# Kernel tuning notes

Measured on AMD Instinct MI355X. Metric: run time of the kernel, lower is better.

Reference implementation:

```python
import jax, jax.numpy as jnp
import numpy as np

PAD, CLS, SEP, UNK = 0, 1, 2, 3
VOCAB, DIM, LATENT = 30000, 768, 5000
B, L, C = 16, 1024, 8


def setup_inputs() -> dict:
    key = jax.random.key(0)
    k1, k2, k3 = jax.random.split(key, 3)
    x = jax.random.randint(k1, (B, L, C), 0, VOCAB, dtype=jnp.int64)
    char_emb = jax.random.normal(k2, (VOCAB, DIM), dtype=jnp.float32)
    latent_mat = jax.random.normal(k3, (LATENT, DIM), dtype=jnp.float32) * (LATENT ** -0.5)
    return {"x": x, "char_emb": char_emb, "latent_mat": latent_mat}


def reference(x, char_emb, latent_mat):
    b, l, c = x.shape
    chars = x.reshape(-1, c)                       # (N, C)
    embs = char_emb[chars]                         # (N, C, D) gather
    pad_mask = chars == PAD                        # (N, C)
    embs = jnp.where(pad_mask[..., None], 0.0, embs)
    summed = embs.sum(axis=1)                      # (N, D)
    counts = jnp.clip((~pad_mask).sum(axis=-1), 1, None)  # (N,)
    lang_emb = jnp.tanh(summed / counts[:, None].astype(summed.dtype))  # (N, D)

    # soft codebook attention: matmul -> softmax -> matmul
    scores = jnp.einsum('nd,kd->nk', lang_emb, latent_mat)   # (N, LATENT)
    dist = jax.nn.softmax(scores, axis=-1)
    latent_emb = jnp.einsum('nk,kd->nd', dist, latent_mat)    # (N, D)
    sde = lang_emb + latent_emb

    # special-token overwrite based on first char id
    first = chars[:, 0]
    for tid in (PAD, UNK, SEP, CLS):
        sde = jnp.where((first == tid)[:, None], char_emb[tid], sde)
    return sde.reshape(b, l, -1)
```

## Files before the change

kernel.cpp:

```cpp
#include <hip/hip_runtime.h>

#define PAD_ID 0
#define NTOK   16384
#define DIM    768
#define KLAT   5000
#define KPAD   5024
#define NSTEP  157
#define TILE_SH 24576
#define TOKB   32

typedef float f32x4 __attribute__((ext_vector_type(4)));
typedef __bf16 bf16x8 __attribute__((ext_vector_type(8)));

__device__ __forceinline__ unsigned short f2bf(float f) {
    unsigned int u = __float_as_uint(f);
    u += 0x7fffu + ((u >> 16) & 1u);
    return (unsigned short)(u >> 16);
}
__device__ __forceinline__ float bf2f(unsigned short h) {
    return __uint_as_float(((unsigned int)h) << 16);
}
__device__ __forceinline__ void async_cp16(const unsigned short* g, unsigned short* l) {
    __builtin_amdgcn_global_load_lds(
        (const __attribute__((address_space(1))) unsigned int*)g,
        (__attribute__((address_space(3))) unsigned int*)l, 16, 0, 0);
}

__global__ __launch_bounds__(256) void cvt_latS(const float* __restrict__ latent,
                                                unsigned short* __restrict__ latbS) {
    int g = blockIdx.x * 256 + threadIdx.x;
    if (g >= NSTEP * 24 * 2 * 64) return;
    int lane = g & 63; int rest = g >> 6;
    int h = rest & 1;  int kfr = rest >> 1;
    int kf = kfr % 24; int t  = kfr / 24;
    int row = t * 32 + h * 16 + (lane & 15);
    int col = kf * 32 + (lane >> 4) * 8;
    float4 v0 = make_float4(0.f,0.f,0.f,0.f), v1 = v0;
    if (row < KLAT) {
        v0 = *(const float4*)(latent + (long)row * DIM + col);
        v1 = *(const float4*)(latent + (long)row * DIM + col + 4);
    }
    uint4 o;
    o.x = (unsigned)f2bf(v0.x) | ((unsigned)f2bf(v0.y) << 16);
    o.y = (unsigned)f2bf(v0.z) | ((unsigned)f2bf(v0.w) << 16);
    o.z = (unsigned)f2bf(v1.x) | ((unsigned)f2bf(v1.y) << 16);
    o.w = (unsigned)f2bf(v1.z) | ((unsigned)f2bf(v1.w) << 16);
    *(uint4*)(latbS + (size_t)g * 8) = o;
}

__global__ __launch_bounds__(256) void cvt_latT(const float* __restrict__ latent,
                                                unsigned short* __restrict__ latbT) {
    int g = blockIdx.x * 256 + threadIdx.x;
    if (g >= NSTEP * DIM * 4) return;
    int kk8 = g & 3; int rest = g >> 2;
    int d = rest % DIM; int t = rest / DIM;
    int kk0 = kk8 * 8;
    unsigned short v[8];
    #pragma unroll
    for (int j = 0; j < 8; ++j) {
        int row = t * 32 + kk0 + j;
        v[j] = (row < KLAT) ? f2bf(latent[(long)row * DIM + d]) : (unsigned short)0;
    }
    *(uint4*)(latbT + (size_t)g * 8) = *(uint4*)v;
}

__global__ __launch_bounds__(192) void build_lang(const int* __restrict__ x,
                                                  const float* __restrict__ cemb,
                                                  unsigned short* __restrict__ langb) {
    int tok = blockIdx.x;
    int t = threadIdx.x;
    const int* xs = x + tok * 8;
    int ids[8]; int cnt = 0;
    #pragma unroll
    for (int c = 0; c < 8; ++c) { ids[c] = xs[c]; cnt += (ids[c] != PAD_ID); }
    float4 acc = make_float4(0.f, 0.f, 0.f, 0.f);
    #pragma unroll
    for (int c = 0; c < 8; ++c) {
        if (ids[c] != PAD_ID) {
            float4 v = *(const float4*)(cemb + (long)ids[c] * DIM + t * 4);
            acc.x += v.x; acc.y += v.y; acc.z += v.z; acc.w += v.w;
        }
    }
    float cntf = (float)max(cnt, 1);
    unsigned int u0 = (unsigned int)f2bf(tanhf(acc.x / cntf)) |
                      ((unsigned int)f2bf(tanhf(acc.y / cntf)) << 16);
    unsigned int u1 = (unsigned int)f2bf(tanhf(acc.z / cntf)) |
                      ((unsigned int)f2bf(tanhf(acc.w / cntf)) << 16);
    *(uint2*)(langb + tok * DIM + t * 4) = make_uint2(u0, u1);
}

__global__ __launch_bounds__(256, 2) void fused_sde(
        const int* __restrict__ x, const float* __restrict__ cemb,
        const unsigned short* __restrict__ langb,
        const unsigned short* __restrict__ latbS,
        const unsigned short* __restrict__ latbT,
        float* __restrict__ out) {
    __shared__ unsigned short sLat[TILE_SH];
    __shared__ unsigned short sP[TOKB * 40];
    __shared__ float sL[2][TOKB];

    const int tid  = threadIdx.x;
    const int w    = tid >> 6;
    const int lane = tid & 63;
    const int ln   = lane & 15;
    const int quad = lane >> 4;
    const int tt   = w & 1;
    const int lt   = w >> 1;
    const int m0   = blockIdx.x * TOKB;

    uint4 qf[24];
    {
        const unsigned short* qr = langb + (m0 + tt * 16 + ln) * DIM;
        #pragma unroll
        for (int kf = 0; kf < 24; ++kf)
            qf[kf] = *(const uint4*)(qr + kf * 32 + quad * 8);
    }

    f32x4 accO[2][12];
    #pragma unroll
    for (int mt = 0; mt < 2; ++mt)
        #pragma unroll
        for (int dt = 0; dt < 12; ++dt)
            accO[mt][dt] = (f32x4){0.f, 0.f, 0.f, 0.f};
    float lpart = 0.f;

    #pragma unroll
    for (int i = 0; i < 12; ++i)
        async_cp16(latbS + ((size_t)i * 256 + tid) * 8,
                   sLat + (i * 256 + (tid & ~63)) * 8);
    __syncthreads();

    const int aBase = lt * 64 + lane;
    const int bBase = (w * 192 + ln) * 32 + quad * 8;

    for (int s = 0; s < NSTEP; ++s) {
        const unsigned short* bt = latbT + (size_t)s * TILE_SH;

        uint4 bO0[4];
        #pragma unroll
        for (int dt = 0; dt < 4; ++dt)
            bO0[dt] = *(const uint4*)(bt + bBase + dt * 512);

        f32x4 sva = {0.f,0.f,0.f,0.f}, svb = {0.f,0.f,0.f,0.f};
        #pragma unroll
        for (int kp = 0; kp < 12; ++kp) {
            bf16x8 a0 = *(const bf16x8*)&sLat[((2 * kp)     * 128 + aBase) * 8];
            bf16x8 a1 = *(const bf16x8*)&sLat[((2 * kp + 1) * 128 + aBase) * 8];
            bf16x8 b0 = *(const bf16x8*)&qf[2 * kp];
            bf16x8 b1 = *(const bf16x8*)&qf[2 * kp + 1];
            sva = __builtin_amdgcn_mfma_f32_16x16x32_bf16(a0, b0, sva, 0, 0, 0);
            svb = __builtin_amdgcn_mfma_f32_16x16x32_bf16(a1, b1, svb, 0, 0, 0);
        }

        uint4 bO1[4];
        #pragma unroll
        for (int dt = 0; dt < 4; ++dt)
            bO1[dt] = *(const uint4*)(bt + bBase + (dt + 4) * 512);

        {
            const int lat0 = s * 32 + lt * 16 + quad * 4;
            f32x4 sv = sva + svb;
            float e0 = (lat0     < KLAT) ? __expf(sv[0]) : 0.f;
            float e1 = (lat0 + 1 < KLAT) ? __expf(sv[1]) : 0.f;
            float e2 = (lat0 + 2 < KLAT) ? __expf(sv[2]) : 0.f;
            float e3 = (lat0 + 3 < KLAT) ? __expf(sv[3]) : 0.f;
            lpart += (e0 + e1) + (e2 + e3);
            unsigned int p01 = (unsigned)f2bf(e0) | ((unsigned)f2bf(e1) << 16);
            unsigned int p23 = (unsigned)f2bf(e2) | ((unsigned)f2bf(e3) << 16);
            *(uint2*)&sP[(tt * 16 + ln) * 40 + lt * 16 + quad * 4] =
                make_uint2(p01, p23);
        }
        __syncthreads();

        bf16x8 pA0 = *(const bf16x8*)&sP[ln * 40 + quad * 8];
        bf16x8 pA1 = *(const bf16x8*)&sP[(16 + ln) * 40 + quad * 8];
        uint4 bO2[4];
        #pragma unroll
        for (int dt = 0; dt < 4; ++dt)
            bO2[dt] = *(const uint4*)(bt + bBase + (dt + 8) * 512);

        {
            int nt = (s + 1 < NSTEP) ? s + 1 : 0;
            const unsigned short* gs = latbS + (size_t)nt * TILE_SH;
            #pragma unroll
            for (int i = 0; i < 12; ++i)
                async_cp16(gs + (i * 256 + tid) * 8,
                           sLat + (i * 256 + (tid & ~63)) * 8);
        }

        #pragma unroll
        for (int dt = 0; dt < 4; ++dt) {
            bf16x8 b = *(const bf16x8*)&bO0[dt];
            accO[0][dt] = __builtin_amdgcn_mfma_f32_16x16x32_bf16(pA0, b, accO[0][dt], 0, 0, 0);
            accO[1][dt] = __builtin_amdgcn_mfma_f32_16x16x32_bf16(pA1, b, accO[1][dt], 0, 0, 0);
        }
        #pragma unroll
        for (int dt = 0; dt < 4; ++dt) {
            bf16x8 b = *(const bf16x8*)&bO1[dt];
            accO[0][dt + 4] = __builtin_amdgcn_mfma_f32_16x16x32_bf16(pA0, b, accO[0][dt + 4], 0, 0, 0);
            accO[1][dt + 4] = __builtin_amdgcn_mfma_f32_16x16x32_bf16(pA1, b, accO[1][dt + 4], 0, 0, 0);
        }
        #pragma unroll
        for (int dt = 0; dt < 4; ++dt) {
            bf16x8 b = *(const bf16x8*)&bO2[dt];
            accO[0][dt + 8] = __builtin_amdgcn_mfma_f32_16x16x32_bf16(pA0, b, accO[0][dt + 8], 0, 0, 0);
            accO[1][dt + 8] = __builtin_amdgcn_mfma_f32_16x16x32_bf16(pA1, b, accO[1][dt + 8], 0, 0, 0);
        }
        __syncthreads();
    }

    lpart += __shfl_xor(lpart, 16, 64);
    lpart += __shfl_xor(lpart, 32, 64);
    if (lane < 16) sL[lt][tt * 16 + lane] = lpart;
    __syncthreads();

    #pragma unroll
    for (int mt = 0; mt < 2; ++mt) {
        int tl0 = mt * 16 + quad * 4;
        float linv[4]; int fid[4];
        #pragma unroll
        for (int r = 0; r < 4; ++r) {
            linv[r] = 1.0f / (sL[0][tl0 + r] + sL[1][tl0 + r]);
            fid[r]  = x[(m0 + tl0 + r) * 8];
        }
        #pragma unroll
        for (int dt = 0; dt < 12; ++dt) {
            int d = w * 192 + dt * 16 + ln;
            #pragma unroll
            for (int r = 0; r < 4; ++r) {
                int tok = m0 + tl0 + r;
                float v = accO[mt][dt][r] * linv[r] + bf2f(langb[tok * DIM + d]);
                if (fid[r] < 4) v = cemb[fid[r] * DIM + d];
                out[tok * DIM + d] = v;
            }
        }
    }
}

extern "C" void kernel_launch(void* const* d_in, const int* in_sizes, int n_in,
                              void* d_out, int out_size, void* d_ws, size_t ws_size,
                              hipStream_t stream) {
    const int*   x      = (const int*)d_in[0];
    const float* cemb   = (const float*)d_in[1];
    const float* latent = (const float*)d_in[2];
    float* out = (float*)d_out;

    unsigned short* langb = (unsigned short*)d_ws;
    unsigned short* latbS = langb + (size_t)NTOK * DIM;
    unsigned short* latbT = latbS + (size_t)NSTEP * TILE_SH;

    int nS = NSTEP * 24 * 2 * 64;
    int nT = NSTEP * DIM * 4;
    cvt_latS<<<(nS + 255) / 256, 256, 0, stream>>>(latent, latbS);
    cvt_latT<<<(nT + 255) / 256, 256, 0, stream>>>(latent, latbT);
    build_lang<<<NTOK, 192, 0, stream>>>(x, cemb, langb);
    fused_sde<<<NTOK / TOKB, 256, 0, stream>>>(x, cemb, langb, latbS, latbT, out);
}
```

Before: 590.3 us.

## Use single padded latent tile in LDS with transpose reads for second GEMM

Replaces the two separately converted latent copies (score layout and a transposed copy streamed from global memory) with one padded bf16 layout staged into LDS per step. The second matmul's B operands are now read from the same LDS tile with ds_read_b64_tr_b16 transpose loads instead of per-step global loads, halving latent conversion work and removing a global read stream from the inner loop. The padding (9 slots per 8 rows) is meant to avoid bank conflicts. In exchange, the LDS tile grows, an explicit lgkmcnt wait and scheduling barrier are added, and correctness depends on the hand-computed transposed addressing.

```diff
diff --git a/kernel.cpp b/kernel.cpp
--- a/kernel.cpp
+++ b/kernel.cpp
@@ -6,16 +6,19 @@
 #define KLAT   5000
 #define KPAD   5024
 #define NSTEP  157
-#define TILE_SH 24576
 #define TOKB   32
+
+#define TILE_SH 26880
+#define TCH     3360
 
 typedef float f32x4 __attribute__((ext_vector_type(4)));
 typedef __bf16 bf16x8 __attribute__((ext_vector_type(8)));
-
-__device__ __forceinline__ unsigned short f2bf(float f) {
+typedef unsigned int u32x2 __attribute__((ext_vector_type(2)));
+
+__device__ __forceinline__ unsigned int f2bf(float f) {
     unsigned int u = __float_as_uint(f);
     u += 0x7fffu + ((u >> 16) & 1u);
-    return (unsigned short)(u >> 16);
+    return u >> 16;
 }
 __device__ __forceinline__ float bf2f(unsigned short h) {
     return __uint_as_float(((unsigned int)h) << 16);
@@ -26,42 +29,26 @@
         (__attribute__((address_space(3))) unsigned int*)l, 16, 0, 0);
 }
 
-__global__ __launch_bounds__(256) void cvt_latS(const float* __restrict__ latent,
-                                                unsigned short* __restrict__ latbS) {
-    int g = blockIdx.x * 256 + threadIdx.x;
-    if (g >= NSTEP * 24 * 2 * 64) return;
-    int lane = g & 63; int rest = g >> 6;
-    int h = rest & 1;  int kfr = rest >> 1;
-    int kf = kfr % 24; int t  = kfr / 24;
-    int row = t * 32 + h * 16 + (lane & 15);
-    int col = kf * 32 + (lane >> 4) * 8;
-    float4 v0 = make_float4(0.f,0.f,0.f,0.f), v1 = v0;
-    if (row < KLAT) {
-        v0 = *(const float4*)(latent + (long)row * DIM + col);
-        v1 = *(const float4*)(latent + (long)row * DIM + col + 4);
-    }
-    uint4 o;
-    o.x = (unsigned)f2bf(v0.x) | ((unsigned)f2bf(v0.y) << 16);
-    o.y = (unsigned)f2bf(v0.z) | ((unsigned)f2bf(v0.w) << 16);
-    o.z = (unsigned)f2bf(v1.x) | ((unsigned)f2bf(v1.y) << 16);
-    o.w = (unsigned)f2bf(v1.z) | ((unsigned)f2bf(v1.w) << 16);
-    *(uint4*)(latbS + (size_t)g * 8) = o;
-}
-
-__global__ __launch_bounds__(256) void cvt_latT(const float* __restrict__ latent,
-                                                unsigned short* __restrict__ latbT) {
-    int g = blockIdx.x * 256 + threadIdx.x;
-    if (g >= NSTEP * DIM * 4) return;
-    int kk8 = g & 3; int rest = g >> 2;
-    int d = rest % DIM; int t = rest / DIM;
-    int kk0 = kk8 * 8;
-    unsigned short v[8];
-    #pragma unroll
-    for (int j = 0; j < 8; ++j) {
-        int row = t * 32 + kk0 + j;
-        v[j] = (row < KLAT) ? f2bf(latent[(long)row * DIM + d]) : (unsigned short)0;
-    }
-    *(uint4*)(latbT + (size_t)g * 8) = *(uint4*)v;
+__global__ __launch_bounds__(256) void cvt_latU(const float* __restrict__ latent,
+                                                unsigned short* __restrict__ latb) {
+    int c = blockIdx.x * 256 + threadIdx.x;
+    if (c >= NSTEP * TCH) return;
+    int t  = c / TCH;  int r  = c - t * TCH;
+    int dG = r / 70;   int cc = r - dG * 70;
+    int slot = cc >> 1; int ln0 = (cc & 1) * 8;
+    int q = slot / 9;  int jj = slot - q * 9;
+    int row = t * 32 + q * 8 + jj;
+    uint4 o = make_uint4(0u, 0u, 0u, 0u);
+    if (jj < 8 && row < KLAT) {
+        const float* src = latent + (long)row * DIM + dG * 16 + ln0;
+        float4 v0 = *(const float4*)src;
+        float4 v1 = *(const float4*)(src + 4);
+        o.x = f2bf(v0.x) | (f2bf(v0.y) << 16);
+        o.y = f2bf(v0.z) | (f2bf(v0.w) << 16);
+        o.z = f2bf(v1.x) | (f2bf(v1.y) << 16);
+        o.w = f2bf(v1.z) | (f2bf(v1.w) << 16);
+    }
+    *(uint4*)(latb + (size_t)c * 8) = o;
 }
 
 __global__ __launch_bounds__(192) void build_lang(const int* __restrict__ x,
@@ -82,18 +69,15 @@
         }
     }
     float cntf = (float)max(cnt, 1);
-    unsigned int u0 = (unsigned int)f2bf(tanhf(acc.x / cntf)) |
-                      ((unsigned int)f2bf(tanhf(acc.y / cntf)) << 16);
-    unsigned int u1 = (unsigned int)f2bf(tanhf(acc.z / cntf)) |
-                      ((unsigned int)f2bf(tanhf(acc.w / cntf)) << 16);
+    unsigned int u0 = f2bf(tanhf(acc.x / cntf)) | (f2bf(tanhf(acc.y / cntf)) << 16);
+    unsigned int u1 = f2bf(tanhf(acc.z / cntf)) | (f2bf(tanhf(acc.w / cntf)) << 16);
     *(uint2*)(langb + tok * DIM + t * 4) = make_uint2(u0, u1);
 }
 
 __global__ __launch_bounds__(256, 2) void fused_sde(
         const int* __restrict__ x, const float* __restrict__ cemb,
         const unsigned short* __restrict__ langb,
-        const unsigned short* __restrict__ latbS,
-        const unsigned short* __restrict__ latbT,
+        const unsigned short* __restrict__ latb,
         float* __restrict__ out) {
     __shared__ unsigned short sLat[TILE_SH];
     __shared__ unsigned short sP[TOKB * 40];
@@ -102,18 +86,18 @@
     const int tid  = threadIdx.x;
     const int w    = tid >> 6;
     const int lane = tid & 63;
-    const int ln   = lane & 15;
-    const int quad = lane >> 4;
+    const int lr   = lane & 15;
+    const int q    = lane >> 4;
     const int tt   = w & 1;
     const int lt   = w >> 1;
     const int m0   = blockIdx.x * TOKB;
 
     uint4 qf[24];
     {
-        const unsigned short* qr = langb + (m0 + tt * 16 + ln) * DIM;
+        const unsigned short* qr = langb + (m0 + tt * 16 + lr) * DIM;
         #pragma unroll
         for (int kf = 0; kf < 24; ++kf)
-            qf[kf] = *(const uint4*)(qr + kf * 32 + quad * 8);
+            qf[kf] = *(const uint4*)(qr + kf * 32 + q * 8);
     }
 
     f32x4 accO[2][12];
@@ -124,87 +108,84 @@
             accO[mt][dt] = (f32x4){0.f, 0.f, 0.f, 0.f};
     float lpart = 0.f;
 
-    #pragma unroll
-    for (int i = 0; i < 12; ++i)
-        async_cp16(latbS + ((size_t)i * 256 + tid) * 8,
-                   sLat + (i * 256 + (tid & ~63)) * 8);
+    const int latg  = lt * 16 + lr;
+    const int slotA = (latg >> 3) * 9 + (latg & 7);
+    const int aBaseE = (q >> 1) * 560 + slotA * 16 + (q & 1) * 8;
+
+    const unsigned sbase =
+        (unsigned)(size_t)(__attribute__((address_space(3))) unsigned short*)sLat;
+    const unsigned bAddr = sbase + (unsigned)(w * 13440 + q * 288 + lr * 2);
+
+    {
+        #pragma unroll
+        for (int i = 0; i < 13; ++i)
+            async_cp16(latb + ((size_t)i * 256 + tid) * 8,
+                       sLat + (i * 256 + (tid & ~63)) * 8);
+        if (tid < 32)
+            async_cp16(latb + ((size_t)13 * 256 + tid) * 8,
+                       sLat + (13 * 256) * 8);
+    }
     __syncthreads();
 
-    const int aBase = lt * 64 + lane;
-    const int bBase = (w * 192 + ln) * 32 + quad * 8;
-
     for (int s = 0; s < NSTEP; ++s) {
-        const unsigned short* bt = latbT + (size_t)s * TILE_SH;
-
-        uint4 bO0[4];
-        #pragma unroll
-        for (int dt = 0; dt < 4; ++dt)
-            bO0[dt] = *(const uint4*)(bt + bBase + dt * 512);
-
         f32x4 sva = {0.f,0.f,0.f,0.f}, svb = {0.f,0.f,0.f,0.f};
         #pragma unroll
         for (int kp = 0; kp < 12; ++kp) {
-            bf16x8 a0 = *(const bf16x8*)&sLat[((2 * kp)     * 128 + aBase) * 8];
-            bf16x8 a1 = *(const bf16x8*)&sLat[((2 * kp + 1) * 128 + aBase) * 8];
+            bf16x8 a0 = *(const bf16x8*)&sLat[aBaseE + (2 * kp)     * 1120];
+            bf16x8 a1 = *(const bf16x8*)&sLat[aBaseE + (2 * kp + 1) * 1120];
             bf16x8 b0 = *(const bf16x8*)&qf[2 * kp];
             bf16x8 b1 = *(const bf16x8*)&qf[2 * kp + 1];
             sva = __builtin_amdgcn_mfma_f32_16x16x32_bf16(a0, b0, sva, 0, 0, 0);
             svb = __builtin_amdgcn_mfma_f32_16x16x32_bf16(a1, b1, svb, 0, 0, 0);
         }
 
-        uint4 bO1[4];
-        #pragma unroll
-        for (int dt = 0; dt < 4; ++dt)
-            bO1[dt] = *(const uint4*)(bt + bBase + (dt + 4) * 512);
+        u32x2 bLo[12], bHi[12];
+        #pragma unroll
+        for (int dt = 0; dt < 12; ++dt) {
+            asm volatile("ds_read_b64_tr_b16 %0, %1 offset:%2"
+                         : "=v"(bLo[dt]) : "v"(bAddr), "i"(dt * 1120));
+            asm volatile("ds_read_b64_tr_b16 %0, %1 offset:%2"
+                         : "=v"(bHi[dt]) : "v"(bAddr), "i"(dt * 1120 + 128));
+        }
 
         {
-            const int lat0 = s * 32 + lt * 16 + quad * 4;
+            const int lat0 = s * 32 + lt * 16 + q * 4;
             f32x4 sv = sva + svb;
             float e0 = (lat0     < KLAT) ? __expf(sv[0]) : 0.f;
             float e1 = (lat0 + 1 < KLAT) ? __expf(sv[1]) : 0.f;
             float e2 = (lat0 + 2 < KLAT) ? __expf(sv[2]) : 0.f;
             float e3 = (lat0 + 3 < KLAT) ? __expf(sv[3]) : 0.f;
             lpart += (e0 + e1) + (e2 + e3);
-            unsigned int p01 = (unsigned)f2bf(e0) | ((unsigned)f2bf(e1) << 16);
-            unsigned int p23 = (unsigned)f2bf(e2) | ((unsigned)f2bf(e3) << 16);
-            *(uint2*)&sP[(tt * 16 + ln) * 40 + lt * 16 + quad * 4] =
+            unsigned int p01 = f2bf(e0) | (f2bf(e1) << 16);
+            unsigned int p23 = f2bf(e2) | (f2bf(e3) << 16);
+            *(uint2*)&sP[(tt * 16 + lr) * 40 + lt * 16 + q * 4] =
                 make_uint2(p01, p23);
         }
+
+        asm volatile("s_waitcnt lgkmcnt(0)" ::: "memory");
+        __builtin_amdgcn_sched_barrier(0);
         __syncthreads();
-
-        bf16x8 pA0 = *(const bf16x8*)&sP[ln * 40 + quad * 8];
-        bf16x8 pA1 = *(const bf16x8*)&sP[(16 + ln) * 40 + quad * 8];
-        uint4 bO2[4];
-        #pragma unroll
-        for (int dt = 0; dt < 4; ++dt)
-            bO2[dt] = *(const uint4*)(bt + bBase + (dt + 8) * 512);
 
         {
             int nt = (s + 1 < NSTEP) ? s + 1 : 0;
-            const unsigned short* gs = latbS + (size_t)nt * TILE_SH;
+            const unsigned short* gs = latb + (size_t)nt * TILE_SH;
             #pragma unroll
-            for (int i = 0; i < 12; ++i)
-                async_cp16(gs + (i * 256 + tid) * 8,
+            for (int i = 0; i < 13; ++i)
+                async_cp16(gs + ((size_t)i * 256 + tid) * 8,
                            sLat + (i * 256 + (tid & ~63)) * 8);
-        }
-
-        #pragma unroll
-        for (int dt = 0; dt < 4; ++dt) {
-            bf16x8 b = *(const bf16x8*)&bO0[dt];
+            if (tid < 32)
+                async_cp16(gs + ((size_t)13 * 256 + tid) * 8,
+                           sLat + (13 * 256) * 8);
+        }
+
+        bf16x8 pA0 = *(const bf16x8*)&sP[lr * 40 + q * 8];
+        bf16x8 pA1 = *(const bf16x8*)&sP[(16 + lr) * 40 + q * 8];
+        #pragma unroll
+        for (int dt = 0; dt < 12; ++dt) {
+            uint4 bw = make_uint4(bLo[dt].x, bLo[dt].y, bHi[dt].x, bHi[dt].y);
+            bf16x8 b = *(bf16x8*)&bw;
             accO[0][dt] = __builtin_amdgcn_mfma_f32_16x16x32_bf16(pA0, b, accO[0][dt], 0, 0, 0);
             accO[1][dt] = __builtin_amdgcn_mfma_f32_16x16x32_bf16(pA1, b, accO[1][dt], 0, 0, 0);
-        }
-        #pragma unroll
-        for (int dt = 0; dt < 4; ++dt) {
-            bf16x8 b = *(const bf16x8*)&bO1[dt];
-            accO[0][dt + 4] = __builtin_amdgcn_mfma_f32_16x16x32_bf16(pA0, b, accO[0][dt + 4], 0, 0, 0);
-            accO[1][dt + 4] = __builtin_amdgcn_mfma_f32_16x16x32_bf16(pA1, b, accO[1][dt + 4], 0, 0, 0);
-        }
-        #pragma unroll
-        for (int dt = 0; dt < 4; ++dt) {
-            bf16x8 b = *(const bf16x8*)&bO2[dt];
-            accO[0][dt + 8] = __builtin_amdgcn_mfma_f32_16x16x32_bf16(pA0, b, accO[0][dt + 8], 0, 0, 0);
-            accO[1][dt + 8] = __builtin_amdgcn_mfma_f32_16x16x32_bf16(pA1, b, accO[1][dt + 8], 0, 0, 0);
         }
         __syncthreads();
     }
@@ -216,7 +197,7 @@
 
     #pragma unroll
     for (int mt = 0; mt < 2; ++mt) {
-        int tl0 = mt * 16 + quad * 4;
+        int tl0 = mt * 16 + q * 4;
         float linv[4]; int fid[4];
         #pragma unroll
         for (int r = 0; r < 4; ++r) {
@@ -225,7 +206,7 @@
         }
         #pragma unroll
         for (int dt = 0; dt < 12; ++dt) {
-            int d = w * 192 + dt * 16 + ln;
+            int d = w * 192 + dt * 16 + lr;
             #pragma unroll
             for (int r = 0; r < 4; ++r) {
                 int tok = m0 + tl0 + r;
@@ -246,13 +227,10 @@
     float* out = (float*)d_out;
 
     unsigned short* langb = (unsigned short*)d_ws;
-    unsigned short* latbS = langb + (size_t)NTOK * DIM;
-    unsigned short* latbT = latbS + (size_t)NSTEP * TILE_SH;
-
-    int nS = NSTEP * 24 * 2 * 64;
-    int nT = NSTEP * DIM * 4;
-    cvt_latS<<<(nS + 255) / 256, 256, 0, stream>>>(latent, latbS);
-    cvt_latT<<<(nT + 255) / 256, 256, 0, stream>>>(latent, latbT);
+    unsigned short* latb  = langb + (size_t)NTOK * DIM;
+
+    int nU = NSTEP * TCH;
+    cvt_latU<<<(nU + 255) / 256, 256, 0, stream>>>(latent, latb);
     build_lang<<<NTOK, 192, 0, stream>>>(x, cemb, langb);
-    fused_sde<<<NTOK / TOKB, 256, 0, stream>>>(x, cemb, langb, latbS, latbT, out);
-}
+    fused_sde<<<NTOK / TOKB, 256, 0, stream>>>(x, cemb, langb, latb, out);
+}
```

New measurement: 657.1 us. +11.3%, slower.

## Double token tile to 64 with 512 threads and double-buffered latent LDS

Applied to the files above, without the earlier changes.

The fused kernel now handles 64 tokens per block with 8 waves, so each latent tile streamed from global memory and LDS is reused across twice as many tokens. The latent score tile and the probability tile are double-buffered in shared memory, which removes the trailing barrier per step and issues the next tile's async copy at the start of the step. It also tidies the bf16 conversion helper. In exchange it uses more LDS and registers per block (accO is 4x6 per wave), and there are half as many blocks, which may reduce occupancy or the number of blocks per CU.

```diff
diff --git a/kernel.cpp b/kernel.cpp
--- a/kernel.cpp
+++ b/kernel.cpp
@@ -7,15 +7,15 @@
 #define KPAD   5024
 #define NSTEP  157
 #define TILE_SH 24576
-#define TOKB   32
+#define TOKB   64
 
 typedef float f32x4 __attribute__((ext_vector_type(4)));
 typedef __bf16 bf16x8 __attribute__((ext_vector_type(8)));
 
-__device__ __forceinline__ unsigned short f2bf(float f) {
+__device__ __forceinline__ unsigned int f2bf(float f) {
     unsigned int u = __float_as_uint(f);
     u += 0x7fffu + ((u >> 16) & 1u);
-    return (unsigned short)(u >> 16);
+    return u >> 16;
 }
 __device__ __forceinline__ float bf2f(unsigned short h) {
     return __uint_as_float(((unsigned int)h) << 16);
@@ -41,10 +41,10 @@
         v1 = *(const float4*)(latent + (long)row * DIM + col + 4);
     }
     uint4 o;
-    o.x = (unsigned)f2bf(v0.x) | ((unsigned)f2bf(v0.y) << 16);
-    o.y = (unsigned)f2bf(v0.z) | ((unsigned)f2bf(v0.w) << 16);
-    o.z = (unsigned)f2bf(v1.x) | ((unsigned)f2bf(v1.y) << 16);
-    o.w = (unsigned)f2bf(v1.z) | ((unsigned)f2bf(v1.w) << 16);
+    o.x = f2bf(v0.x) | (f2bf(v0.y) << 16);
+    o.y = f2bf(v0.z) | (f2bf(v0.w) << 16);
+    o.z = f2bf(v1.x) | (f2bf(v1.y) << 16);
+    o.w = f2bf(v1.z) | (f2bf(v1.w) << 16);
     *(uint4*)(latbS + (size_t)g * 8) = o;
 }
 
@@ -59,7 +59,8 @@
     #pragma unroll
     for (int j = 0; j < 8; ++j) {
         int row = t * 32 + kk0 + j;
-        v[j] = (row < KLAT) ? f2bf(latent[(long)row * DIM + d]) : (unsigned short)0;
+        v[j] = (row < KLAT) ? (unsigned short)f2bf(latent[(long)row * DIM + d])
+                            : (unsigned short)0;
     }
     *(uint4*)(latbT + (size_t)g * 8) = *(uint4*)v;
 }
@@ -82,131 +83,124 @@
         }
     }
     float cntf = (float)max(cnt, 1);
-    unsigned int u0 = (unsigned int)f2bf(tanhf(acc.x / cntf)) |
-                      ((unsigned int)f2bf(tanhf(acc.y / cntf)) << 16);
-    unsigned int u1 = (unsigned int)f2bf(tanhf(acc.z / cntf)) |
-                      ((unsigned int)f2bf(tanhf(acc.w / cntf)) << 16);
+    unsigned int u0 = f2bf(tanhf(acc.x / cntf)) | (f2bf(tanhf(acc.y / cntf)) << 16);
+    unsigned int u1 = f2bf(tanhf(acc.z / cntf)) | (f2bf(tanhf(acc.w / cntf)) << 16);
     *(uint2*)(langb + tok * DIM + t * 4) = make_uint2(u0, u1);
 }
 
-__global__ __launch_bounds__(256, 2) void fused_sde(
+__global__ __launch_bounds__(512, 2) void fused_sde(
         const int* __restrict__ x, const float* __restrict__ cemb,
         const unsigned short* __restrict__ langb,
         const unsigned short* __restrict__ latbS,
         const unsigned short* __restrict__ latbT,
         float* __restrict__ out) {
-    __shared__ unsigned short sLat[TILE_SH];
-    __shared__ unsigned short sP[TOKB * 40];
+    __shared__ unsigned short sLat[2][TILE_SH];
+    __shared__ unsigned short sP[2][TOKB * 40];
     __shared__ float sL[2][TOKB];
 
     const int tid  = threadIdx.x;
     const int w    = tid >> 6;
     const int lane = tid & 63;
-    const int ln   = lane & 15;
-    const int quad = lane >> 4;
-    const int tt   = w & 1;
-    const int lt   = w >> 1;
+    const int lr   = lane & 15;
+    const int q    = lane >> 4;
+    const int tt   = w & 3;
+    const int lt   = w >> 2;
     const int m0   = blockIdx.x * TOKB;
 
     uint4 qf[24];
     {
-        const unsigned short* qr = langb + (m0 + tt * 16 + ln) * DIM;
+        const unsigned short* qr = langb + (m0 + tt * 16 + lr) * DIM;
         #pragma unroll
         for (int kf = 0; kf < 24; ++kf)
-            qf[kf] = *(const uint4*)(qr + kf * 32 + quad * 8);
-    }
-
-    f32x4 accO[2][12];
-    #pragma unroll
-    for (int mt = 0; mt < 2; ++mt)
-        #pragma unroll
-        for (int dt = 0; dt < 12; ++dt)
+            qf[kf] = *(const uint4*)(qr + kf * 32 + q * 8);
+    }
+
+    f32x4 accO[4][6];
+    #pragma unroll
+    for (int mt = 0; mt < 4; ++mt)
+        #pragma unroll
+        for (int dt = 0; dt < 6; ++dt)
             accO[mt][dt] = (f32x4){0.f, 0.f, 0.f, 0.f};
     float lpart = 0.f;
 
-    #pragma unroll
-    for (int i = 0; i < 12; ++i)
-        async_cp16(latbS + ((size_t)i * 256 + tid) * 8,
-                   sLat + (i * 256 + (tid & ~63)) * 8);
+    const int aBase = lt * 64 + lane;
+    const int bBase = (w * 96 + lr) * 32 + q * 8;
+
+    #pragma unroll
+    for (int i = 0; i < 6; ++i)
+        async_cp16(latbS + ((size_t)i * 512 + tid) * 8,
+                   &sLat[0][(i * 512 + (tid & ~63)) * 8]);
     __syncthreads();
 
-    const int aBase = lt * 64 + lane;
-    const int bBase = (w * 192 + ln) * 32 + quad * 8;
-
     for (int s = 0; s < NSTEP; ++s) {
+        const int c = s & 1;
+
+        {
+            int nt = (s + 1 < NSTEP) ? s + 1 : 0;
+            const unsigned short* gs = latbS + (size_t)nt * TILE_SH;
+            #pragma unroll
+            for (int i = 0; i < 6; ++i)
+                async_cp16(gs + ((size_t)i * 512 + tid) * 8,
+                           &sLat[c ^ 1][(i * 512 + (tid & ~63)) * 8]);
+        }
+
         const unsigned short* bt = latbT + (size_t)s * TILE_SH;
-
-        uint4 bO0[4];
-        #pragma unroll
-        for (int dt = 0; dt < 4; ++dt)
+        uint4 bO0[3], bO1[3];
+        #pragma unroll
+        for (int dt = 0; dt < 3; ++dt)
             bO0[dt] = *(const uint4*)(bt + bBase + dt * 512);
 
         f32x4 sva = {0.f,0.f,0.f,0.f}, svb = {0.f,0.f,0.f,0.f};
         #pragma unroll
         for (int kp = 0; kp < 12; ++kp) {
-            bf16x8 a0 = *(const bf16x8*)&sLat[((2 * kp)     * 128 + aBase) * 8];
-            bf16x8 a1 = *(const bf16x8*)&sLat[((2 * kp + 1) * 128 + aBase) * 8];
+            bf16x8 a0 = *(const bf16x8*)&sLat[c][((2 * kp)     * 128 + aBase) * 8];
+            bf16x8 a1 = *(const bf16x8*)&sLat[c][((2 * kp + 1) * 128 + aBase) * 8];
             bf16x8 b0 = *(const bf16x8*)&qf[2 * kp];
             bf16x8 b1 = *(const bf16x8*)&qf[2 * kp + 1];
             sva = __builtin_amdgcn_mfma_f32_16x16x32_bf16(a0, b0, sva, 0, 0, 0);
             svb = __builtin_amdgcn_mfma_f32_16x16x32_bf16(a1, b1, svb, 0, 0, 0);
         }
 
-        uint4 bO1[4];
-        #pragma unroll
-        for (int dt = 0; dt < 4; ++dt)
-            bO1[dt] = *(const uint4*)(bt + bBase + (dt + 4) * 512);
+        #pragma unroll
+        for (int dt = 0; dt < 3; ++dt)
+            bO1[dt] = *(const uint4*)(bt + bBase + (dt + 3) * 512);
 
         {
-            const int lat0 = s * 32 + lt * 16 + quad * 4;
+            const int lat0 = s * 32 + lt * 16 + q * 4;
             f32x4 sv = sva + svb;
             float e0 = (lat0     < KLAT) ? __expf(sv[0]) : 0.f;
             float e1 = (lat0 + 1 < KLAT) ? __expf(sv[1]) : 0.f;
             float e2 = (lat0 + 2 < KLAT) ? __expf(sv[2]) : 0.f;
             float e3 = (lat0 + 3 < KLAT) ? __expf(sv[3]) : 0.f;
             lpart += (e0 + e1) + (e2 + e3);
-            unsigned int p01 = (unsigned)f2bf(e0) | ((unsigned)f2bf(e1) << 16);
-            unsigned int p23 = (unsigned)f2bf(e2) | ((unsigned)f2bf(e3) << 16);
-            *(uint2*)&sP[(tt * 16 + ln) * 40 + lt * 16 + quad * 4] =
+            unsigned int p01 = f2bf(e0) | (f2bf(e1) << 16);
+            unsigned int p23 = f2bf(e2) | (f2bf(e3) << 16);
+            *(uint2*)&sP[c][(tt * 16 + lr) * 40 + lt * 16 + q * 4] =
                 make_uint2(p01, p23);
         }
+
         __syncthreads();
 
-        bf16x8 pA0 = *(const bf16x8*)&sP[ln * 40 + quad * 8];
-        bf16x8 pA1 = *(const bf16x8*)&sP[(16 + ln) * 40 + quad * 8];
-        uint4 bO2[4];
-        #pragma unroll
-        for (int dt = 0; dt < 4; ++dt)
-            bO2[dt] = *(const uint4*)(bt + bBase + (dt + 8) * 512);
-
-        {
-            int nt = (s + 1 < NSTEP) ? s + 1 : 0;
-            const unsigned short* gs = latbS + (size_t)nt * TILE_SH;
-            #pragma unroll
-            for (int i = 0; i < 12; ++i)
-                async_cp16(gs + (i * 256 + tid) * 8,
-                           sLat + (i * 256 + (tid & ~63)) * 8);
-        }
-
-        #pragma unroll
-        for (int dt = 0; dt < 4; ++dt) {
+        bf16x8 pA[4];
+        #pragma unroll
+        for (int mt = 0; mt < 4; ++mt)
+            pA[mt] = *(const bf16x8*)&sP[c][(mt * 16 + lr) * 40 + q * 8];
+        #pragma unroll
+        for (int dt = 0; dt < 3; ++dt) {
             bf16x8 b = *(const bf16x8*)&bO0[dt];
-            accO[0][dt] = __builtin_amdgcn_mfma_f32_16x16x32_bf16(pA0, b, accO[0][dt], 0, 0, 0);
-            accO[1][dt] = __builtin_amdgcn_mfma_f32_16x16x32_bf16(pA1, b, accO[1][dt], 0, 0, 0);
-        }
-        #pragma unroll
-        for (int dt = 0; dt < 4; ++dt) {
+            #pragma unroll
+            for (int mt = 0; mt < 4; ++mt)
+                accO[mt][dt] = __builtin_amdgcn_mfma_f32_16x16x32_bf16(
+                    pA[mt], b, accO[mt][dt], 0, 0, 0);
+        }
+        #pragma unroll
+        for (int dt = 0; dt < 3; ++dt) {
             bf16x8 b = *(const bf16x8*)&bO1[dt];
-            accO[0][dt + 4] = __builtin_amdgcn_mfma_f32_16x16x32_bf16(pA0, b, accO[0][dt + 4], 0, 0, 0);
-            accO[1][dt + 4] = __builtin_amdgcn_mfma_f32_16x16x32_bf16(pA1, b, accO[1][dt + 4], 0, 0, 0);
-        }
-        #pragma unroll
-        for (int dt = 0; dt < 4; ++dt) {
-            bf16x8 b = *(const bf16x8*)&bO2[dt];
-            accO[0][dt + 8] = __builtin_amdgcn_mfma_f32_16x16x32_bf16(pA0, b, accO[0][dt + 8], 0, 0, 0);
-            accO[1][dt + 8] = __builtin_amdgcn_mfma_f32_16x16x32_bf16(pA1, b, accO[1][dt + 8], 0, 0, 0);
-        }
-        __syncthreads();
+            #pragma unroll
+            for (int mt = 0; mt < 4; ++mt)
+                accO[mt][dt + 3] = __builtin_amdgcn_mfma_f32_16x16x32_bf16(
+                    pA[mt], b, accO[mt][dt + 3], 0, 0, 0);
+        }
     }
 
     lpart += __shfl_xor(lpart, 16, 64);
@@ -215,8 +209,8 @@
     __syncthreads();
 
     #pragma unroll
-    for (int mt = 0; mt < 2; ++mt) {
-        int tl0 = mt * 16 + quad * 4;
+    for (int mt = 0; mt < 4; ++mt) {
+        int tl0 = mt * 16 + q * 4;
         float linv[4]; int fid[4];
         #pragma unroll
         for (int r = 0; r < 4; ++r) {
@@ -224,8 +218,8 @@
             fid[r]  = x[(m0 + tl0 + r) * 8];
         }
         #pragma unroll
-        for (int dt = 0; dt < 12; ++dt) {
-            int d = w * 192 + dt * 16 + ln;
+        for (int dt = 0; dt < 6; ++dt) {
+            int d = w * 96 + dt * 16 + lr;
             #pragma unroll
             for (int r = 0; r < 4; ++r) {
                 int tok = m0 + tl0 + r;
@@ -254,5 +248,5 @@
     cvt_latS<<<(nS + 255) / 256, 256, 0, stream>>>(latent, latbS);
     cvt_latT<<<(nT + 255) / 256, 256, 0, stream>>>(latent, latbT);
     build_lang<<<NTOK, 192, 0, stream>>>(x, cemb, langb);
-    fused_sde<<<NTOK / TOKB, 256, 0, stream>>>(x, cemb, langb, latbS, latbT, out);
-}
+    fused_sde<<<NTOK / TOKB, 512, 0, stream>>>(x, cemb, langb, latbS, latbT, out);
+}
```

Measured after the change: 582.8 us. No clear change (-1.3%).
